# Kernel tuning notes

Hardware: AMD Instinct MI355X
Metric: run time of the kernel (lower is better)

The kernel has to match this reference:

```python
import jax, jax.numpy as jnp
import numpy as np

N0, N1, N2 = 200000, 50000, 10000   # source nodes, hop-1 targets, final targets
D, C, DEG = 256, 40, 10


def _sage(x_src, x_tgt, row, col, n_tgt, Wl, Wr, b, reduce):
    # PyG SAGEConv: lin_l(aggr(messages)) + lin_r(x_target); bias on lin_l only
    msg = x_src[row]                                   # [E, D] gather
    if reduce == 'mean':
        s = jax.ops.segment_sum(msg, col, num_segments=n_tgt)
        cnt = jax.ops.segment_sum(jnp.ones((row.shape[0], 1), msg.dtype), col, num_segments=n_tgt)
        agg = s / jnp.maximum(cnt, 1.0)
    else:
        agg = jax.ops.segment_max(msg, col, num_segments=n_tgt)
    return agg @ Wl + b + x_tgt @ Wr


def setup_inputs() -> dict:
    key = jax.random.key(0)
    ks = jax.random.split(key, 16)
    x = jax.random.normal(ks[0], (N0, D), jnp.float32)
    # every target gets exactly DEG sampled neighbors (NeighborSampler-style)
    row0 = jax.random.randint(ks[1], (N1 * DEG,), 0, N0, jnp.int32)
    col0 = jnp.repeat(jnp.arange(N1, dtype=jnp.int32), DEG)
    edge_index0 = jnp.stack([row0, col0])
    row1 = jax.random.randint(ks[2], (N2 * DEG,), 0, N1, jnp.int32)
    col1 = jnp.repeat(jnp.arange(N2, dtype=jnp.int32), DEG)
    edge_index1 = jnp.stack([row1, col1])
    s = 1.0 / np.sqrt(D)
    w = lambda k, shp: jax.random.uniform(k, shp, jnp.float32, -s, s)
    return {
        'x': x, 'edge_index0': edge_index0, 'edge_index1': edge_index1,
        'Wl_m0': w(ks[3], (D, D)), 'Wr_m0': w(ks[4], (D, D)), 'b_m0': jnp.zeros((D,), jnp.float32),
        'Wl_x0': w(ks[5], (D, D)), 'Wr_x0': w(ks[6], (D, D)), 'b_x0': jnp.zeros((D,), jnp.float32),
        'Wl_m1': w(ks[7], (D, D)), 'Wr_m1': w(ks[8], (D, D)), 'b_m1': jnp.zeros((D,), jnp.float32),
        'Wl_x1': w(ks[9], (D, D)), 'Wr_x1': w(ks[10], (D, D)), 'b_x1': jnp.zeros((D,), jnp.float32),
        'W_post': w(ks[11], (2 * D, C)), 'b_post': jnp.zeros((C,), jnp.float32),
    }


def reference(x, edge_index0, edge_index1,
              Wl_m0, Wr_m0, b_m0, Wl_x0, Wr_x0, b_x0,
              Wl_m1, Wr_m1, b_m1, Wl_x1, Wr_x1, b_x1,
              W_post, b_post):
    row0, col0 = edge_index0[0], edge_index0[1]
    row1, col1 = edge_index1[0], edge_index1[1]
    tgt0 = x[:N1]
    h_m = jax.nn.relu(_sage(x, tgt0, row0, col0, N1, Wl_m0, Wr_m0, b_m0, 'mean'))
    h_x = jax.nn.relu(_sage(x, tgt0, row0, col0, N1, Wl_x0, Wr_x0, b_x0, 'max'))
    # NOTE: faithful to source bug: layer-1 target features are the RAW x[:size[1]]
    tgt1 = x[:N2]
    o_m = _sage(h_m, tgt1, row1, col1, N2, Wl_m1, Wr_m1, b_m1, 'mean')
    o_x = _sage(h_x, tgt1, row1, col1, N2, Wl_x1, Wr_x1, b_x1, 'max')
    out = jnp.concatenate([o_m, o_x], axis=-1) @ W_post + b_post
    return jax.nn.log_softmax(out, axis=-1)
```

## Files before the change

kernel.cpp:

```cpp
#include <hip/hip_runtime.h>
#include <hip/hip_bf16.h>
#include <math.h>

#define N0v 200000
#define N1v 50000
#define N2v 10000
#define Dv  256
#define Cv  40
#define DEGv 10

typedef __attribute__((ext_vector_type(8))) short          s16x8;
typedef __attribute__((ext_vector_type(8))) unsigned short u16x8;
typedef __attribute__((ext_vector_type(4))) float          f32x4;

static __device__ __forceinline__ unsigned short f2bf(float f) {
    __hip_bfloat16 h = __float2bfloat16(f);
    return *reinterpret_cast<unsigned short*>(&h);
}
static __device__ __forceinline__ float bf2f(unsigned short u) {
    __hip_bfloat16 h = *reinterpret_cast<__hip_bfloat16*>(&u);
    return __bfloat162float(h);
}

static __device__ __forceinline__ void gload16(const void* g, void* l) {
    __builtin_amdgcn_global_load_lds(
        (const __attribute__((address_space(1))) unsigned int*)g,
        (__attribute__((address_space(3))) unsigned int*)l, 16, 0, 0);
}

__global__ __launch_bounds__(256) void prep_kernel(
    const float* __restrict__ Wl0, const float* __restrict__ Wr0,
    const float* __restrict__ Wl1, const float* __restrict__ Wr1,
    const float* __restrict__ Wl2, const float* __restrict__ Wr2,
    const float* __restrict__ Wl3, const float* __restrict__ Wr3,
    unsigned short* __restrict__ WT0, unsigned short* __restrict__ WT1,
    unsigned short* __restrict__ WT2, unsigned short* __restrict__ WT3)
{
    const int idx = blockIdx.x;
    const int p = idx >> 8;
    const int n = idx & 255;
    const int k = threadIdx.x;
    const float* Wl = (p == 0) ? Wl0 : (p == 1) ? Wl1 : (p == 2) ? Wl2 : Wl3;
    const float* Wr = (p == 0) ? Wr0 : (p == 1) ? Wr1 : (p == 2) ? Wr2 : Wr3;
    unsigned short* WT = (p == 0) ? WT0 : (p == 1) ? WT1 : (p == 2) ? WT2 : WT3;
    WT[(size_t)n * 512 + k]       = f2bf(Wl[(size_t)k * Dv + n]);
    WT[(size_t)n * 512 + 256 + k] = f2bf(Wr[(size_t)k * Dv + n]);
}

__global__ __launch_bounds__(256) void agg0_kernel(
    const float* __restrict__ x, const int* __restrict__ row,
    unsigned short* __restrict__ om, unsigned short* __restrict__ ox,
    unsigned short* __restrict__ xtb)
{
    const int t = blockIdx.x * 4 + (threadIdx.x >> 6);
    const int c = threadIdx.x & 63;
    const int eb = t * DEGv;
    float4 s = make_float4(0.f, 0.f, 0.f, 0.f);
    float4 mx = make_float4(-INFINITY, -INFINITY, -INFINITY, -INFINITY);
#pragma unroll
    for (int k = 0; k < DEGv; ++k) {
        const int r = row[eb + k];
        float4 v = ((const float4*)x)[(size_t)r * 64 + c];
        s.x += v.x; s.y += v.y; s.z += v.z; s.w += v.w;
        mx.x = fmaxf(mx.x, v.x); mx.y = fmaxf(mx.y, v.y);
        mx.z = fmaxf(mx.z, v.z); mx.w = fmaxf(mx.w, v.w);
    }
    const float inv = 1.0f / DEGv;
    unsigned short osum[4] = { f2bf(s.x * inv), f2bf(s.y * inv), f2bf(s.z * inv), f2bf(s.w * inv) };
    unsigned short omax[4] = { f2bf(mx.x), f2bf(mx.y), f2bf(mx.z), f2bf(mx.w) };
    *(uint2*)&om[(size_t)t * Dv + c * 4] = *(uint2*)osum;
    *(uint2*)&ox[(size_t)t * Dv + c * 4] = *(uint2*)omax;

    float4 v = ((const float4*)x)[(size_t)t * 64 + c];
    unsigned short o[4] = { f2bf(v.x), f2bf(v.y), f2bf(v.z), f2bf(v.w) };
    *(uint2*)&xtb[(size_t)t * Dv + c * 4] = *(uint2*)o;
}

__global__ __launch_bounds__(256) void agg1_kernel(
    const unsigned short* __restrict__ hm, const unsigned short* __restrict__ hx,
    const int* __restrict__ row,
    unsigned short* __restrict__ om, unsigned short* __restrict__ ox)
{
    const int t = blockIdx.x * 8 + (threadIdx.x >> 5);
    const int c = threadIdx.x & 31;
    const int eb = t * DEGv;
    float s[8] = {};
    float mx[8] = { -INFINITY, -INFINITY, -INFINITY, -INFINITY,
                    -INFINITY, -INFINITY, -INFINITY, -INFINITY };
#pragma unroll
    for (int k = 0; k < DEGv; ++k) {
        const int r = row[eb + k];
        u16x8 vm = ((const u16x8*)hm)[(size_t)r * 32 + c];
        u16x8 vx = ((const u16x8*)hx)[(size_t)r * 32 + c];
#pragma unroll
        for (int j = 0; j < 8; ++j) {
            s[j]  += bf2f(vm[j]);
            mx[j]  = fmaxf(mx[j], bf2f(vx[j]));
        }
    }
    const float inv = 1.0f / DEGv;
    unsigned short osum[8], omax[8];
#pragma unroll
    for (int j = 0; j < 8; ++j) { osum[j] = f2bf(s[j] * inv); omax[j] = f2bf(mx[j]); }
    *(u16x8*)&om[(size_t)t * Dv + c * 8] = *(u16x8*)osum;
    *(u16x8*)&ox[(size_t)t * Dv + c * 8] = *(u16x8*)omax;
}

template<int RELU, int OUTBF>
__global__ __launch_bounds__(256) void gemm_mfma_kernel(
    const unsigned short* __restrict__ A1a, const unsigned short* __restrict__ A1b,
    const unsigned short* __restrict__ A2,
    const unsigned short* __restrict__ WTa, const unsigned short* __restrict__ WTb,
    const float* __restrict__ biasa, const float* __restrict__ biasb,
    void* outa, void* outb, int M, int ldc, int col_step)
{
    __shared__ unsigned short Asb[128 * 64];
    __shared__ unsigned short Bsb[128 * 64];

    const int z = blockIdx.z;
    const unsigned short* A1 = z ? A1b : A1a;
    const unsigned short* WT = z ? WTb : WTa;
    const float* bias = z ? biasb : biasa;
    void* outp = z ? outb : outa;
    const int col_off = z * col_step;

    const int tid  = threadIdx.x;
    const int lane = tid & 63;
    const int w    = tid >> 6;
    const int wr   = w >> 1, wc = w & 1;
    const int m0   = blockIdx.x * 128, n0 = blockIdx.y * 128;

    const int lrow = lane >> 3;
    const int scol = ((lane & 7) ^ lrow) * 8;

    const unsigned short* pA1[4];
    const unsigned short* pA2[4];
    const unsigned short* pB[4];
    unsigned short* lA[4];
    unsigned short* lB[4];
#pragma unroll
    for (int c = 0; c < 4; ++c) {
        const int r = w * 32 + c * 8 + lrow;
        int gm = m0 + r; if (gm >= M) gm = M - 1;
        pA1[c] = A1 + (size_t)gm * Dv + scol;
        pA2[c] = A2 + (size_t)gm * Dv + scol;
        pB[c]  = WT + (size_t)(n0 + r) * 512 + scol;
        lA[c] = &Asb[(w * 32 + c * 8) * 64];
        lB[c] = &Bsb[(w * 32 + c * 8) * 64];
    }

    const int fr = lane & 15;
    const int f7 = lane & 7;

    f32x4 acc[4][4] = {};

    for (int k0 = 0; k0 < 512; k0 += 64) {
        __syncthreads();
        if (k0 < 256) {
#pragma unroll
            for (int c = 0; c < 4; ++c) gload16(pA1[c] + k0, lA[c]);
        } else {
#pragma unroll
            for (int c = 0; c < 4; ++c) gload16(pA2[c] + (k0 - 256), lA[c]);
        }
#pragma unroll
        for (int c = 0; c < 4; ++c) gload16(pB[c] + k0, lB[c]);
        __syncthreads();

#pragma unroll
        for (int kk = 0; kk < 2; ++kk) {
            const int sl = kk * 4 + (lane >> 4);
            s16x8 af[4], bfr[4];
#pragma unroll
            for (int i = 0; i < 4; ++i) {
                const int ar = wr * 64 + i * 16 + fr;
                af[i]  = *(const s16x8*)&Asb[ar * 64 + ((sl ^ f7) << 3)];
                const int br = wc * 64 + i * 16 + fr;
                bfr[i] = *(const s16x8*)&Bsb[br * 64 + ((sl ^ f7) << 3)];
            }
#pragma unroll
            for (int i = 0; i < 4; ++i)
#pragma unroll
                for (int j = 0; j < 4; ++j)
                    acc[i][j] = __builtin_amdgcn_mfma_f32_16x16x32_bf16(af[i], bfr[j], acc[i][j], 0, 0, 0);
        }
    }

#pragma unroll
    for (int i = 0; i < 4; ++i) {
#pragma unroll
        for (int reg = 0; reg < 4; ++reg) {
            const int gr = m0 + wr * 64 + i * 16 + (lane >> 4) * 4 + reg;
            if (gr < M) {
#pragma unroll
                for (int j = 0; j < 4; ++j) {
                    const int gc = n0 + wc * 64 + j * 16 + fr;
                    float v = acc[i][j][reg] + bias[gc];
                    if (RELU) v = fmaxf(v, 0.0f);
                    if (OUTBF)
                        ((unsigned short*)outp)[(size_t)gr * ldc + col_off + gc] = f2bf(v);
                    else
                        ((float*)outp)[(size_t)gr * ldc + col_off + gc] = v;
                }
            }
        }
    }
}

__global__ __launch_bounds__(256) void post_kernel(
    const unsigned short* __restrict__ ocat, const float* __restrict__ Wp,
    const float* __restrict__ bp, float* __restrict__ out, int nrows)
{
    __shared__ float sW[512 * 40];
    __shared__ float sP[7][32][40];
    __shared__ float sb[Cv];

    const int tid = threadIdx.x;

    for (int i = tid; i < 5120; i += 256)
        ((float4*)sW)[i] = ((const float4*)Wp)[i];
    if (tid < Cv) sb[tid] = bp[tid];
    __syncthreads();

    const int q = tid >> 5;
    const int r = tid & 31;
    const int t = blockIdx.x * 32 + r;
    const bool valid = (t < nrows);

    float acc[Cv] = {};
    if (valid) {
        const unsigned short* prow = ocat + (size_t)t * 512 + q * 64;
        for (int kk = 0; kk < 64; kk += 8) {
            u16x8 v = *(const u16x8*)(prow + kk);
            const float* wbase = &sW[(q * 64 + kk) * Cv];
#pragma unroll
            for (int e = 0; e < 8; ++e) {
                const float xv = bf2f(v[e]);
                const float* wr_ = wbase + e * Cv;
#pragma unroll
                for (int c4 = 0; c4 < Cv; c4 += 4) {
                    f32x4 wv = *(const f32x4*)(wr_ + c4);
                    acc[c4 + 0] += xv * wv[0];
                    acc[c4 + 1] += xv * wv[1];
                    acc[c4 + 2] += xv * wv[2];
                    acc[c4 + 3] += xv * wv[3];
                }
            }
        }
    }

    if (q > 0) {
#pragma unroll
        for (int c4 = 0; c4 < Cv; c4 += 4)
            *(f32x4*)&sP[q - 1][r][c4] = *(f32x4*)&acc[c4];
    }
    __syncthreads();

    if (q == 0 && valid) {
#pragma unroll
        for (int p = 0; p < 7; ++p)
#pragma unroll
            for (int c4 = 0; c4 < Cv; c4 += 4) {
                f32x4 pv = *(const f32x4*)&sP[p][r][c4];
                acc[c4 + 0] += pv[0];
                acc[c4 + 1] += pv[1];
                acc[c4 + 2] += pv[2];
                acc[c4 + 3] += pv[3];
            }
        float m = -INFINITY;
#pragma unroll
        for (int c = 0; c < Cv; ++c) { acc[c] += sb[c]; m = fmaxf(m, acc[c]); }
        float s = 0.0f;
#pragma unroll
        for (int c = 0; c < Cv; ++c) s += expf(acc[c] - m);
        const float lse = m + logf(s);
        float* dst = out + (size_t)t * Cv;
#pragma unroll
        for (int c4 = 0; c4 < Cv; c4 += 4) {
            float o[4] = { acc[c4] - lse, acc[c4 + 1] - lse, acc[c4 + 2] - lse, acc[c4 + 3] - lse };
            *(float4*)(dst + c4) = *(float4*)o;
        }
    }
}

extern "C" void kernel_launch(void* const* d_in, const int* in_sizes, int n_in,
                              void* d_out, int out_size, void* d_ws, size_t ws_size,
                              hipStream_t stream)
{
    const float* x      = (const float*)d_in[0];
    const int*   ei0    = (const int*)d_in[1];
    const int*   ei1    = (const int*)d_in[2];
    const float* Wl_m0  = (const float*)d_in[3];
    const float* Wr_m0  = (const float*)d_in[4];
    const float* b_m0   = (const float*)d_in[5];
    const float* Wl_x0  = (const float*)d_in[6];
    const float* Wr_x0  = (const float*)d_in[7];
    const float* b_x0   = (const float*)d_in[8];
    const float* Wl_m1  = (const float*)d_in[9];
    const float* Wr_m1  = (const float*)d_in[10];
    const float* b_m1   = (const float*)d_in[11];
    const float* Wl_x1  = (const float*)d_in[12];
    const float* Wr_x1  = (const float*)d_in[13];
    const float* b_x1   = (const float*)d_in[14];
    const float* W_post = (const float*)d_in[15];
    const float* b_post = (const float*)d_in[16];
    float* out = (float*)d_out;

    const int* row0 = ei0;
    const int* row1 = ei1;

    char* ws = (char*)d_ws;
    const size_t NB = (size_t)N1v * Dv * 2;
    unsigned short* xtb = (unsigned short*)(ws);
    unsigned short* am  = (unsigned short*)(ws + NB);
    unsigned short* ax  = (unsigned short*)(ws + 2 * NB);
    unsigned short* hm  = (unsigned short*)(ws + 3 * NB);
    unsigned short* hx  = (unsigned short*)(ws + 4 * NB);
    unsigned short* a1m = (unsigned short*)(ws + 5 * NB);
    unsigned short* a1x = a1m + (size_t)N2v * Dv;
    unsigned short* ocat = (unsigned short*)(ws + 5 * NB + (size_t)2 * N2v * Dv * 2);
    unsigned short* WT0m = ocat + (size_t)N2v * 2 * Dv;
    unsigned short* WT0x = WT0m + (size_t)256 * 512;
    unsigned short* WT1m = WT0x + (size_t)256 * 512;
    unsigned short* WT1x = WT1m + (size_t)256 * 512;

    const dim3 blk(256);

    prep_kernel<<<1024, blk, 0, stream>>>(
        Wl_m0, Wr_m0, Wl_x0, Wr_x0, Wl_m1, Wr_m1, Wl_x1, Wr_x1,
        WT0m, WT0x, WT1m, WT1x);
    agg0_kernel<<<N1v / 4, blk, 0, stream>>>(x, row0, am, ax, xtb);

    gemm_mfma_kernel<1, 1><<<dim3((N1v + 127) / 128, 2, 2), blk, 0, stream>>>(
        am, ax, xtb, WT0m, WT0x, b_m0, b_x0, hm, hx, N1v, Dv, 0);

    agg1_kernel<<<N2v / 8, blk, 0, stream>>>(hm, hx, row1, a1m, a1x);
    gemm_mfma_kernel<0, 1><<<dim3((N2v + 127) / 128, 2, 2), blk, 0, stream>>>(
        a1m, a1x, xtb, WT1m, WT1x, b_m1, b_x1, ocat, ocat, N2v, 2 * Dv, Dv);

    post_kernel<<<(N2v + 31) / 32, blk, 0, stream>>>(ocat, W_post, b_post, out, N2v);
}
```

Baseline: 224.8 us.

## Widen GEMM tile to full N and fuse weight prep into aggregation kernel

The GEMM kernel now computes all 256 output columns per block (128x256 tile, 4x8 accumulators per wave), so each A tile is loaded once instead of twice. This halves A-operand global traffic but doubles B LDS and accumulator register use, which may lower occupancy. The weight transpose/convert prep is also merged into the layer-0 aggregation kernel as extra blocks, removing one launch.

```diff
diff --git a/kernel.cpp b/kernel.cpp
--- a/kernel.cpp
+++ b/kernel.cpp
@@ -28,7 +28,10 @@
         (__attribute__((address_space(3))) unsigned int*)l, 16, 0, 0);
 }
 
-__global__ __launch_bounds__(256) void prep_kernel(
+__global__ __launch_bounds__(256) void agg0_prep_kernel(
+    const float* __restrict__ x, const int* __restrict__ row,
+    unsigned short* __restrict__ om, unsigned short* __restrict__ ox,
+    unsigned short* __restrict__ xtb,
     const float* __restrict__ Wl0, const float* __restrict__ Wr0,
     const float* __restrict__ Wl1, const float* __restrict__ Wr1,
     const float* __restrict__ Wl2, const float* __restrict__ Wr2,
@@ -36,44 +39,41 @@
     unsigned short* __restrict__ WT0, unsigned short* __restrict__ WT1,
     unsigned short* __restrict__ WT2, unsigned short* __restrict__ WT3)
 {
-    const int idx = blockIdx.x;
-    const int p = idx >> 8;
-    const int n = idx & 255;
-    const int k = threadIdx.x;
-    const float* Wl = (p == 0) ? Wl0 : (p == 1) ? Wl1 : (p == 2) ? Wl2 : Wl3;
-    const float* Wr = (p == 0) ? Wr0 : (p == 1) ? Wr1 : (p == 2) ? Wr2 : Wr3;
-    unsigned short* WT = (p == 0) ? WT0 : (p == 1) ? WT1 : (p == 2) ? WT2 : WT3;
-    WT[(size_t)n * 512 + k]       = f2bf(Wl[(size_t)k * Dv + n]);
-    WT[(size_t)n * 512 + 256 + k] = f2bf(Wr[(size_t)k * Dv + n]);
-}
-
-__global__ __launch_bounds__(256) void agg0_kernel(
-    const float* __restrict__ x, const int* __restrict__ row,
-    unsigned short* __restrict__ om, unsigned short* __restrict__ ox,
-    unsigned short* __restrict__ xtb)
-{
-    const int t = blockIdx.x * 4 + (threadIdx.x >> 6);
-    const int c = threadIdx.x & 63;
-    const int eb = t * DEGv;
-    float4 s = make_float4(0.f, 0.f, 0.f, 0.f);
-    float4 mx = make_float4(-INFINITY, -INFINITY, -INFINITY, -INFINITY);
-#pragma unroll
-    for (int k = 0; k < DEGv; ++k) {
-        const int r = row[eb + k];
-        float4 v = ((const float4*)x)[(size_t)r * 64 + c];
-        s.x += v.x; s.y += v.y; s.z += v.z; s.w += v.w;
-        mx.x = fmaxf(mx.x, v.x); mx.y = fmaxf(mx.y, v.y);
-        mx.z = fmaxf(mx.z, v.z); mx.w = fmaxf(mx.w, v.w);
-    }
-    const float inv = 1.0f / DEGv;
-    unsigned short osum[4] = { f2bf(s.x * inv), f2bf(s.y * inv), f2bf(s.z * inv), f2bf(s.w * inv) };
-    unsigned short omax[4] = { f2bf(mx.x), f2bf(mx.y), f2bf(mx.z), f2bf(mx.w) };
-    *(uint2*)&om[(size_t)t * Dv + c * 4] = *(uint2*)osum;
-    *(uint2*)&ox[(size_t)t * Dv + c * 4] = *(uint2*)omax;
-
-    float4 v = ((const float4*)x)[(size_t)t * 64 + c];
-    unsigned short o[4] = { f2bf(v.x), f2bf(v.y), f2bf(v.z), f2bf(v.w) };
-    *(uint2*)&xtb[(size_t)t * Dv + c * 4] = *(uint2*)o;
+    const int b = blockIdx.x;
+    if (b < 12500) {
+        const int t = b * 4 + (threadIdx.x >> 6);
+        const int c = threadIdx.x & 63;
+        const int eb = t * DEGv;
+        float4 s = make_float4(0.f, 0.f, 0.f, 0.f);
+        float4 mx = make_float4(-INFINITY, -INFINITY, -INFINITY, -INFINITY);
+#pragma unroll
+        for (int k = 0; k < DEGv; ++k) {
+            const int r = row[eb + k];
+            float4 v = ((const float4*)x)[(size_t)r * 64 + c];
+            s.x += v.x; s.y += v.y; s.z += v.z; s.w += v.w;
+            mx.x = fmaxf(mx.x, v.x); mx.y = fmaxf(mx.y, v.y);
+            mx.z = fmaxf(mx.z, v.z); mx.w = fmaxf(mx.w, v.w);
+        }
+        const float inv = 1.0f / DEGv;
+        unsigned short osum[4] = { f2bf(s.x * inv), f2bf(s.y * inv), f2bf(s.z * inv), f2bf(s.w * inv) };
+        unsigned short omax[4] = { f2bf(mx.x), f2bf(mx.y), f2bf(mx.z), f2bf(mx.w) };
+        *(uint2*)&om[(size_t)t * Dv + c * 4] = *(uint2*)osum;
+        *(uint2*)&ox[(size_t)t * Dv + c * 4] = *(uint2*)omax;
+
+        float4 v = ((const float4*)x)[(size_t)t * 64 + c];
+        unsigned short o[4] = { f2bf(v.x), f2bf(v.y), f2bf(v.z), f2bf(v.w) };
+        *(uint2*)&xtb[(size_t)t * Dv + c * 4] = *(uint2*)o;
+    } else {
+        const int idx = b - 12500;
+        const int p = idx >> 8;
+        const int n = idx & 255;
+        const int k = threadIdx.x;
+        const float* Wl = (p == 0) ? Wl0 : (p == 1) ? Wl1 : (p == 2) ? Wl2 : Wl3;
+        const float* Wr = (p == 0) ? Wr0 : (p == 1) ? Wr1 : (p == 2) ? Wr2 : Wr3;
+        unsigned short* WT = (p == 0) ? WT0 : (p == 1) ? WT1 : (p == 2) ? WT2 : WT3;
+        WT[(size_t)n * 512 + k]       = f2bf(Wl[(size_t)k * Dv + n]);
+        WT[(size_t)n * 512 + 256 + k] = f2bf(Wr[(size_t)k * Dv + n]);
+    }
 }
 
 __global__ __launch_bounds__(256) void agg1_kernel(
@@ -115,7 +115,7 @@
     void* outa, void* outb, int M, int ldc, int col_step)
 {
     __shared__ unsigned short Asb[128 * 64];
-    __shared__ unsigned short Bsb[128 * 64];
+    __shared__ unsigned short Bsb[256 * 64];
 
     const int z = blockIdx.z;
     const unsigned short* A1 = z ? A1b : A1a;
@@ -127,32 +127,37 @@
     const int tid  = threadIdx.x;
     const int lane = tid & 63;
     const int w    = tid >> 6;
-    const int wr   = w >> 1, wc = w & 1;
-    const int m0   = blockIdx.x * 128, n0 = blockIdx.y * 128;
+    const int wrow = w >> 1;
+    const int wcol = w & 1;
+    const int m0   = blockIdx.x * 128;
 
     const int lrow = lane >> 3;
     const int scol = ((lane & 7) ^ lrow) * 8;
 
     const unsigned short* pA1[4];
     const unsigned short* pA2[4];
-    const unsigned short* pB[4];
     unsigned short* lA[4];
-    unsigned short* lB[4];
 #pragma unroll
     for (int c = 0; c < 4; ++c) {
         const int r = w * 32 + c * 8 + lrow;
         int gm = m0 + r; if (gm >= M) gm = M - 1;
         pA1[c] = A1 + (size_t)gm * Dv + scol;
         pA2[c] = A2 + (size_t)gm * Dv + scol;
-        pB[c]  = WT + (size_t)(n0 + r) * 512 + scol;
         lA[c] = &Asb[(w * 32 + c * 8) * 64];
-        lB[c] = &Bsb[(w * 32 + c * 8) * 64];
+    }
+    const unsigned short* pB[8];
+    unsigned short* lB[8];
+#pragma unroll
+    for (int c = 0; c < 8; ++c) {
+        const int r = w * 64 + c * 8 + lrow;
+        pB[c] = WT + (size_t)r * 512 + scol;
+        lB[c] = &Bsb[(w * 64 + c * 8) * 64];
     }
 
     const int fr = lane & 15;
     const int f7 = lane & 7;
 
-    f32x4 acc[4][4] = {};
+    f32x4 acc[4][8] = {};
 
     for (int k0 = 0; k0 < 512; k0 += 64) {
         __syncthreads();
@@ -164,25 +169,24 @@
             for (int c = 0; c < 4; ++c) gload16(pA2[c] + (k0 - 256), lA[c]);
         }
 #pragma unroll
-        for (int c = 0; c < 4; ++c) gload16(pB[c] + k0, lB[c]);
+        for (int c = 0; c < 8; ++c) gload16(pB[c] + k0, lB[c]);
         __syncthreads();
 
 #pragma unroll
         for (int kk = 0; kk < 2; ++kk) {
             const int sl = kk * 4 + (lane >> 4);
-            s16x8 af[4], bfr[4];
-#pragma unroll
-            for (int i = 0; i < 4; ++i) {
-                const int ar = wr * 64 + i * 16 + fr;
-                af[i]  = *(const s16x8*)&Asb[ar * 64 + ((sl ^ f7) << 3)];
-                const int br = wc * 64 + i * 16 + fr;
-                bfr[i] = *(const s16x8*)&Bsb[br * 64 + ((sl ^ f7) << 3)];
+            const int so = ((sl ^ f7) << 3);
+            s16x8 af[4];
+#pragma unroll
+            for (int i = 0; i < 4; ++i)
+                af[i] = *(const s16x8*)&Asb[(wrow * 64 + i * 16 + fr) * 64 + so];
+#pragma unroll
+            for (int j = 0; j < 8; ++j) {
+                s16x8 bv = *(const s16x8*)&Bsb[(wcol * 128 + j * 16 + fr) * 64 + so];
+#pragma unroll
+                for (int i = 0; i < 4; ++i)
+                    acc[i][j] = __builtin_amdgcn_mfma_f32_16x16x32_bf16(af[i], bv, acc[i][j], 0, 0, 0);
             }
-#pragma unroll
-            for (int i = 0; i < 4; ++i)
-#pragma unroll
-                for (int j = 0; j < 4; ++j)
-                    acc[i][j] = __builtin_amdgcn_mfma_f32_16x16x32_bf16(af[i], bfr[j], acc[i][j], 0, 0, 0);
         }
     }
 
@@ -190,11 +194,11 @@
     for (int i = 0; i < 4; ++i) {
 #pragma unroll
         for (int reg = 0; reg < 4; ++reg) {
-            const int gr = m0 + wr * 64 + i * 16 + (lane >> 4) * 4 + reg;
+            const int gr = m0 + wrow * 64 + i * 16 + (lane >> 4) * 4 + reg;
             if (gr < M) {
 #pragma unroll
-                for (int j = 0; j < 4; ++j) {
-                    const int gc = n0 + wc * 64 + j * 16 + fr;
+                for (int j = 0; j < 8; ++j) {
+                    const int gc = wcol * 128 + j * 16 + fr;
                     float v = acc[i][j][reg] + bias[gc];
                     if (RELU) v = fmaxf(v, 0.0f);
                     if (OUTBF)
@@ -326,16 +330,16 @@
 
     const dim3 blk(256);
 
-    prep_kernel<<<1024, blk, 0, stream>>>(
+    agg0_prep_kernel<<<12500 + 1024, blk, 0, stream>>>(
+        x, row0, am, ax, xtb,
         Wl_m0, Wr_m0, Wl_x0, Wr_x0, Wl_m1, Wr_m1, Wl_x1, Wr_x1,
         WT0m, WT0x, WT1m, WT1x);
-    agg0_kernel<<<N1v / 4, blk, 0, stream>>>(x, row0, am, ax, xtb);
-
-    gemm_mfma_kernel<1, 1><<<dim3((N1v + 127) / 128, 2, 2), blk, 0, stream>>>(
+
+    gemm_mfma_kernel<1, 1><<<dim3((N1v + 127) / 128, 1, 2), blk, 0, stream>>>(
         am, ax, xtb, WT0m, WT0x, b_m0, b_x0, hm, hx, N1v, Dv, 0);
 
     agg1_kernel<<<N2v / 8, blk, 0, stream>>>(hm, hx, row1, a1m, a1x);
-    gemm_mfma_kernel<0, 1><<<dim3((N2v + 127) / 128, 2, 2), blk, 0, stream>>>(
+    gemm_mfma_kernel<0, 1><<<dim3((N2v + 127) / 128, 1, 2), blk, 0, stream>>>(
         a1m, a1x, xtb, WT1m, WT1x, b_m1, b_x1, ocat, ocat, N2v, 2 * Dv, Dv);
 
     post_kernel<<<(N2v + 31) / 32, blk, 0, stream>>>(ocat, W_post, b_post, out, N2v);
```

Measured after the change: 217.7 us. -3.2%, faster.
